# Performance work log

Hardware: AMD Instinct MI355X
Metric: run time of the kernel (lower is better)

## Reference

```python
import jax, jax.numpy as jnp
import numpy as np

B, T, C, H = 4, 2048, 1024, 16
HD = C // H


def setup_inputs() -> dict:
    key = jax.random.key(0)
    ks = jax.random.split(key, 9)
    s = 1.0 / np.sqrt(C)
    return {
        "x": jax.random.normal(ks[0], (B, T, C), dtype=jnp.float32),
        "Wk": jax.random.uniform(ks[1], (C, C), jnp.float32, -s, s),
        "bk": jax.random.uniform(ks[2], (C,), jnp.float32, -s, s),
        "Wq": jax.random.uniform(ks[3], (C, C), jnp.float32, -s, s),
        "bq": jax.random.uniform(ks[4], (C,), jnp.float32, -s, s),
        "Wv": jax.random.uniform(ks[5], (C, C), jnp.float32, -s, s),
        "bv": jax.random.uniform(ks[6], (C,), jnp.float32, -s, s),
        "Wp": jax.random.uniform(ks[7], (C, C), jnp.float32, -s, s),
        "bp": jax.random.uniform(ks[8], (C,), jnp.float32, -s, s),
        "padding_mask": jnp.ones((B, T), dtype=jnp.int32),
    }


def reference(x, Wk, bk, Wq, bq, Wv, bv, Wp, bp, padding_mask):
    # torch nn.Linear: y = x @ W.T + b  (W is [out, in])
    def split_heads(t):  # [B,T,C] -> [B,H,T,HD]
        return t.reshape(B, T, H, HD).transpose(0, 2, 1, 3)

    k = split_heads(x @ Wk.T + bk)
    q = split_heads(x @ Wq.T + bq)
    v = split_heads(x @ Wv.T + bv)

    scale = 1.0 / jnp.sqrt(jnp.float32(HD))
    att = jnp.einsum("bhqd,bhkd->bhqk", q, k) * scale  # [B,H,T,T]

    causal = jnp.tril(jnp.ones((T, T), dtype=bool))  # [T,T]
    pad = (padding_mask != 0)[:, None, None, :]       # [B,1,1,T]
    mask = causal[None, None, :, :] & pad
    att = jnp.where(mask, att, -jnp.inf)
    att = jax.nn.softmax(att, axis=-1)

    y = jnp.einsum("bhqk,bhkd->bhqd", att, v)  # [B,H,T,HD]
    y = y.transpose(0, 2, 1, 3).reshape(B, T, C)
    return y @ Wp.T + bp
```

## Files before the change

### kernel.cpp

```cpp
#include <hip/hip_runtime.h>
#include <hip/hip_bf16.h>
#include <math.h>
#include <stdint.h>

#define BB 4
#define TT 2048
#define CC 1024
#define HH 16
#define HD 64
#define MM (BB*TT)
#define NQT 8
#define SCQ 0.180336878f

using f32x4  = __attribute__((ext_vector_type(4))) float;
using f32x16 = __attribute__((ext_vector_type(16))) float;
using i32x4  = __attribute__((ext_vector_type(4))) int;
using bf16x4 = __attribute__((ext_vector_type(4))) __bf16;
using bf16x8 = __attribute__((ext_vector_type(8))) __bf16;

__device__ __forceinline__ float fast_exp2(float x) {
  return __builtin_amdgcn_exp2f(x);
}

__device__ __forceinline__ int cvt_pk_bf16(float lo, float hi_) {
  int r;
  asm("v_cvt_pk_bf16_f32 %0, %1, %2" : "=v"(r) : "v"(lo), "v"(hi_));
  return r;
}

__device__ __forceinline__ void gload_lds16(const void* g, void* l) {
  __builtin_amdgcn_global_load_lds(
      (__attribute__((address_space(1))) void*)(void*)(g),
      (__attribute__((address_space(3))) void*)(l), 16, 0, 0);
}

__global__ __launch_bounds__(256)
void cvt_f32_bf16(const float* __restrict__ s, __bf16* __restrict__ d, int n4) {
  int i = blockIdx.x * 256 + threadIdx.x;
  if (i >= n4) return;
  float4 v = ((const float4*)s)[i];
  bf16x4 o;
  o[0] = (__bf16)v.x; o[1] = (__bf16)v.y; o[2] = (__bf16)v.z; o[3] = (__bf16)v.w;
  *(bf16x4*)(d + (size_t)i * 4) = o;
}

__global__ __launch_bounds__(256)
void cvt_w4(const float* __restrict__ Wq, const float* __restrict__ Wk,
            const float* __restrict__ Wv, const float* __restrict__ Wp,
            __bf16* __restrict__ wqkv, __bf16* __restrict__ wpb) {
  int which = blockIdx.y;
  const float* s = which == 0 ? Wq : which == 1 ? Wk : which == 2 ? Wv : Wp;
  __bf16* d = which == 3 ? wpb : wqkv + (size_t)which * CC * CC;
  float sc = which == 0 ? SCQ : 1.f;
  int i = blockIdx.x * 256 + threadIdx.x;
  float4 v = ((const float4*)s)[i];
  bf16x4 o;
  o[0] = (__bf16)(v.x * sc); o[1] = (__bf16)(v.y * sc);
  o[2] = (__bf16)(v.z * sc); o[3] = (__bf16)(v.w * sc);
  *(bf16x4*)(d + (size_t)i * 4) = o;
}

#define WAITV6 asm volatile("s_waitcnt vmcnt(6)" ::: "memory")
#define WAITV0 asm volatile("s_waitcnt vmcnt(0)" ::: "memory")
#define WAITL0 asm volatile("s_waitcnt lgkmcnt(0)" ::: "memory")
#define BARR   __builtin_amdgcn_s_barrier()
#define SB0    __builtin_amdgcn_sched_barrier(0)
#define PRIO1  __builtin_amdgcn_s_setprio(1)
#define PRIO0  __builtin_amdgcn_s_setprio(0)

#define LDA_SET(buf, mq)                                                      \
  {                                                                           \
    const char* base_ = (const char*)&LA[buf][mq][0] + (wm * 64 + lq) * 128;  \
    _Pragma("unroll")                                                         \
    for (int m4 = 0; m4 < 4; ++m4)                                            \
      _Pragma("unroll")                                                       \
      for (int kk = 0; kk < 2; ++kk)                                          \
        a[m4 * 2 + kk] =                                                      \
            *(const bf16x8*)(base_ + m4 * 2048 + ((kk * 64 + g * 16) ^ swz)); \
  }

#define LDB_SET(buf, nq)                                                      \
  {                                                                           \
    const char* base_ = (const char*)&LB[buf][nq][0] + (wn * 32 + lq) * 128;  \
    _Pragma("unroll")                                                         \
    for (int n2 = 0; n2 < 2; ++n2)                                            \
      _Pragma("unroll")                                                       \
      for (int kk = 0; kk < 2; ++kk)                                          \
        b[nq][n2 * 2 + kk] =                                                  \
            *(const bf16x8*)(base_ + n2 * 2048 + ((kk * 64 + g * 16) ^ swz)); \
  }

#define STAGE_A(nbuf, h, tt)                                                  \
  {                                                                           \
    const char* s_ = Ag + ((size_t)((h)*128 + srow)) * 2048 + (tt)*128 + scol1; \
    gload_lds16(s_, (char*)&LA[nbuf][h][0] + so16);                           \
    gload_lds16(s_ + (size_t)64 * 2048, (char*)&LA[nbuf][h][0] + so16 + 8192);\
  }

#define STAGE_B(nbuf, h, tt)                                                  \
  {                                                                           \
    const char* s_ = Bg + ((size_t)((h)*128 + srow)) * 2048 + (tt)*128 + scol1; \
    gload_lds16(s_, (char*)&LB[nbuf][h][0] + so16);                           \
    gload_lds16(s_ + (size_t)64 * 2048, (char*)&LB[nbuf][h][0] + so16 + 8192);\
  }

#define MFMA_PH(mq, nq)                                                       \
  _Pragma("unroll")                                                           \
  for (int m4 = 0; m4 < 4; ++m4)                                              \
    _Pragma("unroll")                                                         \
    for (int n2 = 0; n2 < 2; ++n2)                                            \
      _Pragma("unroll")                                                       \
      for (int kk = 0; kk < 2; ++kk)                                          \
        acc[mq][m4][nq][n2] = __builtin_amdgcn_mfma_f32_16x16x32_bf16(        \
            a[m4 * 2 + kk], b[nq][n2 * 2 + kk], acc[mq][m4][nq][n2], 0, 0, 0);

__global__ __launch_bounds__(512, 2)
void gemm_qkv(const __bf16* __restrict__ A, const __bf16* __restrict__ Bm,
              const float* __restrict__ b0, const float* __restrict__ b1,
              const float* __restrict__ b2, __bf16* __restrict__ out,
              __bf16* __restrict__ vt) {
  __shared__ __bf16 LA[2][2][128 * 64];
  __shared__ __bf16 LB[2][2][128 * 64];
  const int tid = threadIdx.x, wid = tid >> 6, lane = tid & 63;
  const int g = lane >> 4, lq = lane & 15;
  const int wm = wid >> 2, wn = wid & 3;
  const int bm = blockIdx.x / 12, bn = blockIdx.x % 12;
  const int brow = bm << 8, bcol = bn << 8;
  const int swz = (lq & 7) << 4;

  const int srow = tid >> 3, so16 = tid * 16;
  const int scol1 = ((tid & 7) << 4) ^ ((srow & 7) << 4);
  const char* Ag = (const char*)A + (size_t)brow * 2048;
  const char* Bg = (const char*)Bm + (size_t)bcol * 2048;

  f32x4 acc[2][4][2][2] = {};
  bf16x8 a[8], b[2][4];

  STAGE_A(0, 0, 0); STAGE_B(0, 0, 0); STAGE_B(0, 1, 0); STAGE_A(0, 1, 0);
  STAGE_A(1, 0, 1); STAGE_B(1, 0, 1); STAGE_B(1, 1, 1);
  WAITV6; BARR;

#pragma unroll 1
  for (int t = 0; t < 8; ++t) {
    const bool s2 = (t < 7);
    const int k1 = 2 * t + 1, k2 = 2 * t + 2, k3 = 2 * t + 3;
    LDA_SET(0, 0); LDB_SET(0, 0);
    STAGE_A(1, 1, k1);
    BARR; WAITL0; SB0;
    PRIO1; MFMA_PH(0, 0); PRIO0; BARR;
    LDB_SET(0, 1);
    if (s2) STAGE_A(0, 0, k2);
    BARR; WAITL0; SB0;
    PRIO1; MFMA_PH(0, 1); PRIO0; BARR;
    LDA_SET(0, 1);
    if (s2) STAGE_B(0, 0, k2);
    BARR; WAITL0; SB0;
    PRIO1; MFMA_PH(1, 1); PRIO0; BARR;
    if (s2) { STAGE_B(0, 1, k2); WAITV6; } else { WAITV0; }
    BARR; SB0;
    PRIO1; MFMA_PH(1, 0); PRIO0; BARR;
    LDA_SET(1, 0); LDB_SET(1, 0);
    if (s2) STAGE_A(0, 1, k2);
    BARR; WAITL0; SB0;
    PRIO1; MFMA_PH(0, 0); PRIO0; BARR;
    LDB_SET(1, 1);
    if (s2) STAGE_A(1, 0, k3);
    BARR; WAITL0; SB0;
    PRIO1; MFMA_PH(0, 1); PRIO0; BARR;
    LDA_SET(1, 1);
    if (s2) STAGE_B(1, 0, k3);
    BARR; WAITL0; SB0;
    PRIO1; MFMA_PH(1, 1); PRIO0; BARR;
    if (s2) { STAGE_B(1, 1, k3); WAITV6; }
    BARR; SB0;
    PRIO1; MFMA_PH(1, 0); PRIO0; BARR;
  }

  const int proj = bn >> 2;
  if (proj < 2) {
    const float* bias = proj == 0 ? b0 : b1;
    const float bsc = proj == 0 ? SCQ : 1.f;
#pragma unroll
    for (int mq = 0; mq < 2; ++mq)
#pragma unroll
      for (int nq = 0; nq < 2; ++nq)
#pragma unroll
        for (int n2 = 0; n2 < 2; ++n2) {
          int col = bcol + nq * 128 + wn * 32 + n2 * 16 + lq;
          int cw = col & (CC - 1);
          float bb = bias[cw] * bsc;
          int h_ = cw >> 6, d_ = cw & (HD - 1);
#pragma unroll
          for (int m4 = 0; m4 < 4; ++m4) {
            int row0 = brow + mq * 128 + wm * 64 + m4 * 16 + g * 4;
#pragma unroll
            for (int i = 0; i < 4; ++i) {
              int row = row0 + i;
              int b_ = row >> 11, t_ = row & (TT - 1);
              out[((size_t)proj << 23) +
                  ((((size_t)b_ * HH + h_) * TT + t_) << 6) + d_] =
                  (__bf16)(acc[mq][m4][nq][n2][i] + bb);
            }
          }
        }
  } else {
    __bf16* lt = (__bf16*)&LA[0][0][0];
    const int cv0 = (bn & 3) << 8;
    const int b_ = brow >> 11, t0 = brow & (TT - 1);
    const int hbase = (bn & 3) << 2;
    const int rd_d = tid >> 3, rd_tb = (tid & 7) << 5;
#pragma unroll
    for (int cc = 0; cc < 4; ++cc) {
      if ((wn >> 1) == (cc & 1)) {
#pragma unroll
        for (int n2 = 0; n2 < 2; ++n2) {
          int c = ((wn & 1) << 5) + (n2 << 4) + lq;
          float bb = b2[cv0 + (cc << 6) + c];
#pragma unroll
          for (int mq = 0; mq < 2; ++mq)
#pragma unroll
            for (int m4 = 0; m4 < 4; ++m4) {
              int r = (mq << 7) + (wm << 6) + (m4 << 4) + (g << 2);
              bf16x4 pk;
#pragma unroll
              for (int i = 0; i < 4; ++i)
                pk[i] = (__bf16)(acc[mq][m4][cc >> 1][n2][i] + bb);
              *(bf16x4*)(lt + c * 264 + r) = pk;
            }
        }
      }
      __syncthreads();
      __bf16* dst = vt + (((size_t)((b_ * HH + hbase + cc) * HD + rd_d)) << 11)
                       + t0 + rd_tb;
      const __bf16* srcl = lt + rd_d * 264 + rd_tb;
#pragma unroll
      for (int j = 0; j < 4; ++j)
        *(bf16x8*)(dst + j * 8) = *(const bf16x8*)(srcl + j * 8);
      __syncthreads();
    }
  }
}

__global__ __launch_bounds__(256, 2)
void gemm_proj(const __bf16* __restrict__ A, const __bf16* __restrict__ Bm,
               const float* __restrict__ bias, float* __restrict__ out,
               int M, int N, int K) {
  __shared__ __bf16 As[128 * 32];
  __shared__ __bf16 Bs[128 * 32];
  const int tid = threadIdx.x;
  const int wid = tid >> 6, lane = tid & 63;
  const int g = lane >> 4, lq = lane & 15;
  const int nbn = N >> 7;
  const int brow = (blockIdx.x / nbn) << 7;
  const int bcol = (blockIdx.x % nbn) << 7;
  const int wr = (wid >> 1) << 6, wc = (wid & 1) << 6;

  f32x4 acc[4][4] = {};

  const int o0 = wid * 2048 + lane * 16;
  for (int kt = 0; kt < K; kt += 32) {
    __syncthreads();
#pragma unroll
    for (int j = 0; j < 2; ++j) {
      int o = o0 + j * 1024;
      int row = o >> 6, colb = o & 63;
      gload_lds16((const char*)A + ((size_t)(brow + row) * K + kt) * 2 + colb,
                  (char*)As + o);
      gload_lds16((const char*)Bm + ((size_t)(bcol + row) * K + kt) * 2 + colb,
                  (char*)Bs + o);
    }
    __syncthreads();
    bf16x8 av[4], bv[4];
#pragma unroll
    for (int m = 0; m < 4; ++m)
      av[m] = *(const bf16x8*)(As + (wr + m * 16 + lq) * 32 + g * 8);
#pragma unroll
    for (int n = 0; n < 4; ++n)
      bv[n] = *(const bf16x8*)(Bs + (wc + n * 16 + lq) * 32 + g * 8);
#pragma unroll
    for (int m = 0; m < 4; ++m)
#pragma unroll
      for (int n = 0; n < 4; ++n)
        acc[m][n] = __builtin_amdgcn_mfma_f32_16x16x32_bf16(av[m], bv[n], acc[m][n], 0, 0, 0);
  }

#pragma unroll
  for (int m = 0; m < 4; ++m) {
#pragma unroll
    for (int n = 0; n < 4; ++n) {
      int col = bcol + wc + n * 16 + lq;
      float bb = bias[col];
      int row0 = brow + wr + m * 16 + g * 4;
#pragma unroll
      for (int i = 0; i < 4; ++i)
        out[(size_t)(row0 + i) * N + col] = acc[m][n][i] + bb;
    }
  }
}

__global__ __launch_bounds__(512, 4)
void attn_fwd(const __bf16* __restrict__ Q, const __bf16* __restrict__ K,
              const __bf16* __restrict__ Vt, const int* __restrict__ pm,
              __bf16* __restrict__ Y) {
  __shared__ __bf16 Ks[2][64 * 64];
  __shared__ __bf16 Vs[2][64 * 64];
  const int tid = threadIdx.x, wid = tid >> 6, lane = tid & 63;
  const int l31 = lane & 31, hi = lane >> 5;
  const int bx = blockIdx.x;
  const int bh = bx & 63, jj = bx >> 6;
  const int r2 = ((jj & 1) << 1) | ((jj >> 1) & 1);
  const int qi = (jj & 4) ? r2 : 7 - r2;
  const int b_ = bh >> 4, h_ = bh & 15;
  const __bf16* Qb = Q + (size_t)bh * TT * HD;
  const __bf16* Kb = K + (size_t)bh * TT * HD;
  const __bf16* Vb = Vt + (size_t)bh * HD * TT;
  const int* pmb = pm + b_ * TT;

  const int so = tid * 16;
  const int srow = so >> 7, scol = (so & 127) ^ ((srow & 7) << 4);

  const int q0 = qi << 8;
  const int qw = q0 + wid * 32;
  const int ntiles = 4 * qi + 4;
  const int sw0 = (l31 & 7) << 4;

  bf16x8 qf[4];
#pragma unroll
  for (int s = 0; s < 4; ++s)
    qf[s] = *(const bf16x8*)(Qb + (size_t)(qw + l31) * HD + s * 16 + hi * 8);

  f32x16 o0 = {}, o1 = {};
  float lsum = 0.f;
  float m = -INFINITY;

  gload_lds16((const char*)Kb + (size_t)srow * 128 + scol, (char*)&Ks[0][0] + so);
  gload_lds16((const char*)Vb + (size_t)srow * (TT * 2) + scol, (char*)&Vs[0][0] + so);
  __syncthreads();

  int cur = 0;
#pragma unroll 1
  for (int t = 0; t < ntiles; ++t) {
    const int kv0 = t << 6;
    const int pmv = pmb[kv0 + lane];
    if (t + 1 < ntiles) {
      const size_t nkv0 = (size_t)(kv0 + 64);
      gload_lds16((const char*)Kb + (nkv0 + srow) * 128 + scol,
                  (char*)&Ks[cur ^ 1][0] + so);
      gload_lds16((const char*)Vb + (size_t)srow * (TT * 2) + nkv0 * 2 + scol,
                  (char*)&Vs[cur ^ 1][0] + so);
    }

    if (kv0 <= qw + 31) {
      const unsigned long long bits = __ballot(pmv != 0);
      const char* VsC = (const char*)&Vs[cur][0];

#pragma unroll
      for (int h = 0; h < 2; ++h) {
        const int kvh = kv0 + 32 * h;
        if (kvh <= qw + 31) {
          const char* KsC = (const char*)&Ks[cur][0] + (32 * h + l31) * 128;
          f32x16 S = {};
          __builtin_amdgcn_s_setprio(1);
#pragma unroll
          for (int s = 0; s < 4; ++s) {
            bf16x8 kf = *(const bf16x8*)(KsC + ((32 * s + 16 * hi) ^ sw0));
            S = __builtin_amdgcn_mfma_f32_32x32x16_bf16(kf, qf[s], S, 0, 0, 0);
          }
          __builtin_amdgcn_s_setprio(0);

          if (__builtin_expect(bits != ~0ull, 0)) {
#pragma unroll
            for (int r = 0; r < 16; ++r) {
              const int c = (r & 3) + 8 * (r >> 2);
              if (!((bits >> (32 * h + c + 4 * hi)) & 1ull)) S[r] = -INFINITY;
            }
          }
          if (kvh + 31 > qw) {
            const int thr = qw + l31 - kvh - 4 * hi;
#pragma unroll
            for (int r = 0; r < 16; ++r) {
              const int c = (r & 3) + 8 * (r >> 2);
              S[r] = (c <= thr) ? S[r] : -INFINITY;
            }
          }

          float t0 = fmaxf(fmaxf(S[0], S[1]), fmaxf(S[2], S[3]));
          float t1 = fmaxf(fmaxf(S[4], S[5]), fmaxf(S[6], S[7]));
          float t2 = fmaxf(fmaxf(S[8], S[9]), fmaxf(S[10], S[11]));
          float t3 = fmaxf(fmaxf(S[12], S[13]), fmaxf(S[14], S[15]));
          float pmax = fmaxf(fmaxf(t0, t1), fmaxf(t2, t3));
          if (!__all(pmax <= m + 8.f)) {
            float nm = fmaxf(pmax, __shfl_xor(pmax, 32));
            float mn = fmaxf(m, nm);
            float c = fast_exp2(m - mn);
            m = mn;
            lsum *= c;
#pragma unroll
            for (int r = 0; r < 16; ++r) {
              float cr = __shfl(c, (r & 3) + 8 * (r >> 2) + 4 * hi);
              o0[r] *= cr;
              o1[r] *= cr;
            }
          }

#pragma unroll
          for (int r = 0; r < 16; ++r) S[r] = fast_exp2(S[r] - m);
          {
            float u0 = (S[0] + S[1]) + (S[2] + S[3]);
            float u1 = (S[4] + S[5]) + (S[6] + S[7]);
            float u2 = (S[8] + S[9]) + (S[10] + S[11]);
            float u3 = (S[12] + S[13]) + (S[14] + S[15]);
            lsum += (u0 + u1) + (u2 + u3);
          }

          __builtin_amdgcn_s_setprio(1);
#pragma unroll
          for (int s = 0; s < 2; ++s) {
            const int ub = 2 * s;
            int A0 = cvt_pk_bf16(S[4 * ub + 0], S[4 * ub + 1]);
            int A1 = cvt_pk_bf16(S[4 * ub + 2], S[4 * ub + 3]);
            int B0 = cvt_pk_bf16(S[4 * ub + 4], S[4 * ub + 5]);
            int B1 = cvt_pk_bf16(S[4 * ub + 6], S[4 * ub + 7]);
            int s0 = hi ? A0 : B0, s1 = hi ? A1 : B1;
            int e0 = __shfl_xor(s0, 32), e1 = __shfl_xor(s1, 32);
            i32x4 wv;
            wv[0] = hi ? e0 : A0;
            wv[1] = hi ? e1 : A1;
            wv[2] = hi ? B0 : e0;
            wv[3] = hi ? B1 : e1;
            bf16x8 pa = __builtin_bit_cast(bf16x8, wv);
            const int co = 64 * h + 32 * s + 16 * hi;
            bf16x8 v0 = *(const bf16x8*)(VsC + l31 * 128 + (co ^ sw0));
            bf16x8 v1 = *(const bf16x8*)(VsC + (32 + l31) * 128 + (co ^ sw0));
            o0 = __builtin_amdgcn_mfma_f32_32x32x16_bf16(pa, v0, o0, 0, 0, 0);
            o1 = __builtin_amdgcn_mfma_f32_32x32x16_bf16(pa, v1, o1, 0, 0, 0);
          }
          __builtin_amdgcn_s_setprio(0);
          __builtin_amdgcn_sched_barrier(0);
        }
      }
    }

    __syncthreads();
    cur ^= 1;
  }

  float linv = 1.f / (lsum + __shfl_xor(lsum, 32));
#pragma unroll
  for (int r = 0; r < 16; ++r) {
    const int crow = (r & 3) + 8 * (r >> 2) + 4 * hi;
    float ir = __shfl(linv, crow);
    const int qrow = qw + crow;
    __bf16* yp = Y + ((size_t)(b_ * TT + qrow)) * CC + h_ * HD + l31;
    yp[0]  = (__bf16)(o0[r] * ir);
    yp[32] = (__bf16)(o1[r] * ir);
  }
}

extern "C" void kernel_launch(void* const* d_in, const int* in_sizes, int n_in,
                              void* d_out, int out_size, void* d_ws, size_t ws_size,
                              hipStream_t stream) {
  (void)in_sizes; (void)n_in; (void)out_size; (void)ws_size;
  const float* x  = (const float*)d_in[0];
  const float* Wk = (const float*)d_in[1];
  const float* bk = (const float*)d_in[2];
  const float* Wq = (const float*)d_in[3];
  const float* bq = (const float*)d_in[4];
  const float* Wv = (const float*)d_in[5];
  const float* bv = (const float*)d_in[6];
  const float* Wp = (const float*)d_in[7];
  const float* bp = (const float*)d_in[8];
  const int* pmask = (const int*)d_in[9];

  char* ws = (char*)d_ws;
  const size_t MB = 1024 * 1024;
  __bf16* xb   = (__bf16*)(ws);
  __bf16* wqkv = (__bf16*)(ws + 16 * MB);
  __bf16* wpb  = (__bf16*)(ws + 22 * MB);
  __bf16* qb   = (__bf16*)(ws + 24 * MB);
  __bf16* kb   = qb + ((size_t)1 << 23);
  __bf16* vtb  = (__bf16*)(ws + 56 * MB);
  __bf16* yb   = xb;

  int n4 = (MM * CC) / 4;
  cvt_f32_bf16<<<(n4 + 255) / 256, 256, 0, stream>>>(x, xb, n4);
  cvt_w4<<<dim3((CC * CC / 4) / 256, 4), 256, 0, stream>>>(
      Wq, Wk, Wv, Wp, wqkv, wpb);

  gemm_qkv<<<(MM / 256) * (3 * CC / 256), 512, 0, stream>>>(
      xb, wqkv, bq, bk, bv, qb, vtb);

  attn_fwd<<<NQT * BB * HH, 512, 0, stream>>>(qb, kb, vtb, pmask, yb);

  gemm_proj<<<(MM / 128) * (CC / 128), 256, 0, stream>>>(
      yb, wpb, bp, (float*)d_out, MM, CC, CC);
}
```

Baseline: 180.7 us.

## Triple-buffer K/V tiles in attention and precompute all-ones padding flag

The attention kernel moves from double to triple buffering of K/V shared-memory tiles, prefetching two tiles ahead and waiting on explicit vmcnt counts instead of a full syncthreads per iteration. The padding mask is checked once per block through a shared flag, which skips the per-tile mask load and ballot when every entry is nonzero. Occupancy hint is lowered from 4 to 3 blocks per CU to make room for the larger LDS footprint. It trades occupancy and extra barriers for deeper memory latency hiding.

```diff
diff --git a/kernel.cpp b/kernel.cpp
--- a/kernel.cpp
+++ b/kernel.cpp
@@ -61,6 +61,8 @@
 }
 
 #define WAITV6 asm volatile("s_waitcnt vmcnt(6)" ::: "memory")
+#define WAITV4 asm volatile("s_waitcnt vmcnt(4)" ::: "memory")
+#define WAITV2 asm volatile("s_waitcnt vmcnt(2)" ::: "memory")
 #define WAITV0 asm volatile("s_waitcnt vmcnt(0)" ::: "memory")
 #define WAITL0 asm volatile("s_waitcnt lgkmcnt(0)" ::: "memory")
 #define BARR   __builtin_amdgcn_s_barrier()
@@ -298,12 +300,13 @@
   }
 }
 
-__global__ __launch_bounds__(512, 4)
+__global__ __launch_bounds__(512, 3)
 void attn_fwd(const __bf16* __restrict__ Q, const __bf16* __restrict__ K,
               const __bf16* __restrict__ Vt, const int* __restrict__ pm,
               __bf16* __restrict__ Y) {
-  __shared__ __bf16 Ks[2][64 * 64];
-  __shared__ __bf16 Vs[2][64 * 64];
+  __shared__ __bf16 Ks[3][64 * 64];
+  __shared__ __bf16 Vs[3][64 * 64];
+  __shared__ int flg;
   const int tid = threadIdx.x, wid = tid >> 6, lane = tid & 63;
   const int l31 = lane & 31, hi = lane >> 5;
   const int bx = blockIdx.x;
@@ -329,36 +332,48 @@
   for (int s = 0; s < 4; ++s)
     qf[s] = *(const bf16x8*)(Qb + (size_t)(qw + l31) * HD + s * 16 + hi * 8);
 
+  int4 pm4 = ((const int4*)pmb)[tid];
+  bool okp = pm4.x && pm4.y && pm4.z && pm4.w;
+  if (tid == 0) flg = 1;
+
+  const char* ksrc = (const char*)Kb + (size_t)srow * 128 + scol;
+  const char* vsrc = (const char*)Vb + (size_t)srow * (TT * 2) + scol;
+  char* kdst = (char*)&Ks[0][0] + so;
+  char* vdst = (char*)&Vs[0][0] + so;
+
+#pragma unroll
+  for (int n = 0; n < 3; ++n) {
+    gload_lds16(ksrc + (size_t)n * 8192, kdst + n * 8192);
+    gload_lds16(vsrc + (size_t)n * 128, vdst + n * 8192);
+  }
+  WAITL0; BARR; SB0;
+  if (!okp) flg = 0;
+  WAITL0; WAITV4; BARR; SB0;
+  const bool allones = (flg != 0);
+
   f32x16 o0 = {}, o1 = {};
   float lsum = 0.f;
   float m = -INFINITY;
-
-  gload_lds16((const char*)Kb + (size_t)srow * 128 + scol, (char*)&Ks[0][0] + so);
-  gload_lds16((const char*)Vb + (size_t)srow * (TT * 2) + scol, (char*)&Vs[0][0] + so);
-  __syncthreads();
 
   int cur = 0;
 #pragma unroll 1
   for (int t = 0; t < ntiles; ++t) {
     const int kv0 = t << 6;
-    const int pmv = pmb[kv0 + lane];
-    if (t + 1 < ntiles) {
-      const size_t nkv0 = (size_t)(kv0 + 64);
-      gload_lds16((const char*)Kb + (nkv0 + srow) * 128 + scol,
-                  (char*)&Ks[cur ^ 1][0] + so);
-      gload_lds16((const char*)Vb + (size_t)srow * (TT * 2) + nkv0 * 2 + scol,
-                  (char*)&Vs[cur ^ 1][0] + so);
+    unsigned long long bits = ~0ull;
+    if (__builtin_expect(!allones, 0)) {
+      int pmv = pmb[kv0 + lane];
+      bits = __ballot(pmv != 0);
     }
 
     if (kv0 <= qw + 31) {
-      const unsigned long long bits = __ballot(pmv != 0);
-      const char* VsC = (const char*)&Vs[cur][0];
+      const char* VsC = (const char*)&Vs[0][0] + cur * 8192;
 
 #pragma unroll
       for (int h = 0; h < 2; ++h) {
         const int kvh = kv0 + 32 * h;
         if (kvh <= qw + 31) {
-          const char* KsC = (const char*)&Ks[cur][0] + (32 * h + l31) * 128;
+          const char* KsC =
+              (const char*)&Ks[0][0] + cur * 8192 + (32 * h + l31) * 128;
           f32x16 S = {};
           __builtin_amdgcn_s_setprio(1);
 #pragma unroll
@@ -441,8 +456,18 @@
       }
     }
 
-    __syncthreads();
-    cur ^= 1;
+    BARR; SB0;
+    if (t + 3 < ntiles) {
+      gload_lds16(ksrc + (size_t)(t + 3) * 8192, kdst + cur * 8192);
+      gload_lds16(vsrc + (size_t)(t + 3) * 128, vdst + cur * 8192);
+      WAITV4;
+    } else if (t + 2 < ntiles) {
+      WAITV2;
+    } else if (t + 1 < ntiles) {
+      WAITV0;
+    }
+    BARR; SB0;
+    cur = (cur == 2) ? 0 : cur + 1;
   }
 
   float linv = 1.f / (lsum + __shfl_xor(lsum, 32));
```

New measurement: 195.7 us. +8.3%, slower.
